# Optimization experiments

Measured on AMD Instinct MI355X. Metric: run time of the kernel, lower is better.

Reference implementation:

```python
import jax, jax.numpy as jnp
import numpy as np

USER_NUM = 100000
ITEM_NUM = 50000
E = 128   # embedding_size
A = 64    # attention_size
M = 8     # memory_size
B = 4096  # batch
NF = 50   # friends per user


def _l2norm(x, axis):
    # torch F.normalize(p=2): x / max(||x||, eps)
    n = jnp.sqrt(jnp.sum(x * x, axis=axis, keepdims=True))
    return x / jnp.maximum(n, 1e-12)


def setup_inputs() -> dict:
    key = jax.random.key(0)
    ks = jax.random.split(key, 9)
    u = lambda k, shape: jax.random.uniform(k, shape, jnp.float32, -0.1, 0.1)
    return {
        "input_u": jax.random.randint(ks[0], (B,), 0, USER_NUM),
        "input_i": jax.random.randint(ks[1], (B,), 0, ITEM_NUM),
        "input_uf": jax.random.randint(ks[2], (B, NF), 0, USER_NUM + 1),
        "uidW": u(ks[3], (USER_NUM + 1, E)),
        "iidW": u(ks[4], (ITEM_NUM, E)),
        "i_bias": jnp.zeros((ITEM_NUM,), jnp.float32),
        "Key": u(ks[5], (E, M)),
        "Mem": jnp.ones((M, E), jnp.float32),
        "WA": u(ks[6], (E, A)),
        "BA": jnp.zeros((A,), jnp.float32),
        "U_omega": u(ks[7], (A, 1)),
    }


def reference(input_u, input_i, input_uf, uidW, iidW, i_bias, Key, Mem, WA, BA, U_omega):
    user_num = uidW.shape[0] - 1  # padding id
    uid = uidW[input_u]                      # [B, E]
    iid = iidW[input_i]                      # [B, E]
    i_b = i_bias[input_i]                    # [B]
    fe = uidW[input_uf]                      # [B, F, E] friend embeddings
    fn = (input_uf != user_num).astype(uid.dtype)  # [B, F] valid-friend mask

    fe = fn[:, :, None] * fe
    uid_n = _l2norm(uid, axis=1)
    fe_n = _l2norm(fe, axis=2)
    cross = uid_n[:, None, :] * fe_n                     # [B, F, E]
    att_key = jnp.einsum('bfe,em->bfm', cross, Key)      # [B, F, M]
    att_mem = jax.nn.softmax(att_key, axis=0)            # softmax over batch (faithful to dim=0)
    att_mem = fn[:, :, None] * att_mem
    f1 = jnp.einsum('bfm,me->bfe', att_mem, Mem)         # [B, F, E]
    f2 = f1 * fe
    h = jax.nn.relu(jnp.einsum('bfe,ea->bfa', f2, WA) + BA)
    j = jnp.exp(jnp.einsum('bfa,ao->bfo', h, U_omega))   # [B, F, 1]
    j = fn[:, :, None] * j
    w = j / (jnp.sum(j, axis=1, keepdims=True) + 1e-8)
    friend = jnp.sum(w * f2, axis=1)                     # [B, E] (dropout p=0 -> identity)
    user = uid + friend
    score = jnp.sum(user * iid, axis=1) + i_b            # [B]
    return score
```

## Files before the change

kernel.cpp:

```cpp
#include <hip/hip_runtime.h>

#define EDIM 128
#define MDIM 8
#define ADIM 64
#define NFR  50
#define NCOL (NFR * MDIM)
#define NSLICE 64

typedef __attribute__((ext_vector_type(8))) short short8;
typedef __attribute__((ext_vector_type(4))) float f32x4;

__device__ __forceinline__ float waveReduceSum(float v) {
    #pragma unroll
    for (int s = 32; s >= 1; s >>= 1) v += __shfl_xor(v, s, 64);
    return v;
}
__device__ __forceinline__ short f2bf(float x) {
    unsigned u = __float_as_uint(x);
    u += 0x7FFFu + ((u >> 16) & 1u);
    return (short)(u >> 16);
}
__device__ __forceinline__ float bf2f(short s) {
    return __uint_as_float(((unsigned)(unsigned short)s) << 16);
}
__device__ __forceinline__ int fragOff(int r, int e) {
    int q = (e >> 3) & 3;
    int slot = (q * 16 + (r & 15)) ^ (q << 1);
    int block = ((r >> 4) << 2) | (e >> 5);
    return (block * 64 + slot) * 8;
}
__device__ __forceinline__ int slotR(int l) { return l ^ (((l >> 4) & 3) << 1); }

__global__ __launch_bounds__(256)
void k0_prep(const float* __restrict__ WA, const float* __restrict__ Key,
             short* __restrict__ WAfrag, short* __restrict__ Keyfrag,
             float* __restrict__ Ssum)
{
    int t = blockIdx.x * 256 + threadIdx.x;
    for (int i = t; i < NSLICE * NCOL; i += 5 * 256) Ssum[i] = 0.f;
    if (t < 1024) {
        int lane = t & 63;
        int Kt = (t >> 6) & 3;
        int Nt = t >> 8;
        int n  = Nt * 16 + (lane & 15);
        int k0 = Kt * 32 + (lane >> 4) * 8;
        short8 v;
        #pragma unroll
        for (int j = 0; j < 8; ++j) v[j] = f2bf(WA[(size_t)(k0 + j) * ADIM + n]);
        *(short8*)(WAfrag + (size_t)t * 8) = v;
    } else if (t < 1280) {
        int i = t - 1024;
        int lane = i & 63;
        int Kt = i >> 6;
        int n  = lane & 15;
        int k0 = Kt * 32 + (lane >> 4) * 8;
        short8 v;
        #pragma unroll
        for (int j = 0; j < 8; ++j)
            v[j] = (n < MDIM) ? f2bf(Key[(size_t)(k0 + j) * MDIM + n]) : (short)0;
        *(short8*)(Keyfrag + (size_t)i * 8) = v;
    }
}

__global__ __launch_bounds__(256, 2)
void k1_attkey(const int* __restrict__ input_u, const int* __restrict__ input_uf,
               const float* __restrict__ uidW, const short* __restrict__ Keyfrag,
               float* __restrict__ att_key, float* __restrict__ Ssum,
               int user_num, int B)
{
    __shared__ short crossF4[4][64 * EDIM];
    __shared__ float uidn4[4][EDIM];
    const int w = threadIdx.x >> 6, l = threadIdx.x & 63;
    const int b = blockIdx.x * 4 + w;
    if (b >= B) return;
    short* cF = crossF4[w];
    float* uidn = uidn4[w];

    const int u = input_u[b];
    int ufv = (l < NFR) ? input_uf[(size_t)b * NFR + l] : user_num;
    float x0 = uidW[(size_t)u * EDIM + l];
    float x1 = uidW[(size_t)u * EDIM + 64 + l];
    float s = waveReduceSum(x0 * x0 + x1 * x1);
    float uinv = 1.0f / fmaxf(sqrtf(s), 1e-12f);
    uidn[l] = x0 * uinv;
    uidn[64 + l] = x1 * uinv;
    __builtin_amdgcn_wave_barrier();

    const int kg = l & 15, fl = l >> 4;
    const int e0 = kg * 8;
    float4 un0 = *(const float4*)&uidn[e0];
    float4 un1 = *(const float4*)&uidn[e0 + 4];

    #pragma unroll 4
    for (int it = 0; it < 13; ++it) {
        int f = fl + 4 * it;
        short8 outv = {0, 0, 0, 0, 0, 0, 0, 0};
        if (f < NFR) {
            int fid = __shfl(ufv, f, 64);
            float fn = (fid != user_num) ? 1.f : 0.f;
            const float* fp = uidW + (size_t)fid * EDIM + e0;
            float4 g0 = *(const float4*)fp;
            float4 g1 = *(const float4*)(fp + 4);
            g0.x *= fn; g0.y *= fn; g0.z *= fn; g0.w *= fn;
            g1.x *= fn; g1.y *= fn; g1.z *= fn; g1.w *= fn;
            float fss = g0.x*g0.x + g0.y*g0.y + g0.z*g0.z + g0.w*g0.w
                      + g1.x*g1.x + g1.y*g1.y + g1.z*g1.z + g1.w*g1.w;
            fss += __shfl_xor(fss, 1, 64);
            fss += __shfl_xor(fss, 2, 64);
            fss += __shfl_xor(fss, 4, 64);
            fss += __shfl_xor(fss, 8, 64);
            float inv = 1.0f / fmaxf(sqrtf(fss), 1e-12f);
            outv[0] = f2bf(un0.x * g0.x * inv);
            outv[1] = f2bf(un0.y * g0.y * inv);
            outv[2] = f2bf(un0.z * g0.z * inv);
            outv[3] = f2bf(un0.w * g0.w * inv);
            outv[4] = f2bf(un1.x * g1.x * inv);
            outv[5] = f2bf(un1.y * g1.y * inv);
            outv[6] = f2bf(un1.z * g1.z * inv);
            outv[7] = f2bf(un1.w * g1.w * inv);
        }
        *(short8*)&cF[fragOff(f, e0)] = outv;
    }
    __builtin_amdgcn_wave_barrier();

    const int sl = slotR(l);
    f32x4 acc[4];
    #pragma unroll
    for (int Mt = 0; Mt < 4; ++Mt) acc[Mt] = (f32x4){0.f, 0.f, 0.f, 0.f};
    #pragma unroll
    for (int Kt = 0; Kt < 4; ++Kt) {
        short8 bf = *(const short8*)(Keyfrag + (size_t)(Kt * 64 + l) * 8);
        #pragma unroll
        for (int Mt = 0; Mt < 4; ++Mt) {
            short8 a = *(const short8*)&cF[(((Mt << 2) | Kt) * 64 + sl) * 8];
            acc[Mt] = __builtin_amdgcn_mfma_f32_16x16x32_bf16(a, bf, acc[Mt], 0, 0, 0);
        }
    }
    const int m = l & 15;
    if (m < MDIM) {
        float* Ss = Ssum + (size_t)(b & (NSLICE - 1)) * NCOL;
        #pragma unroll
        for (int Mt = 0; Mt < 4; ++Mt) {
            const int fbase = Mt * 16 + (l >> 4) * 4;
            #pragma unroll
            for (int r = 0; r < 4; ++r) {
                int f = fbase + r;
                if (f < NFR) {
                    att_key[((size_t)b * NFR + f) * MDIM + m] = acc[Mt][r];
                    atomicAdd(&Ss[f * MDIM + m], __expf(acc[Mt][r]));
                }
            }
        }
    }
}

__global__ __launch_bounds__(256)
void k2b_merge(const float* __restrict__ Ssum, float* __restrict__ ise)
{
    int col = blockIdx.x * 256 + threadIdx.x;
    if (col >= NCOL) return;
    float S = 0.f;
    #pragma unroll
    for (int s = 0; s < NSLICE; ++s) S += Ssum[s * NCOL + col];
    ise[col] = 1.0f / S;
}

__global__ __launch_bounds__(256, 2)
void k3_final(const int* __restrict__ input_u, const int* __restrict__ input_i,
              const int* __restrict__ input_uf, const float* __restrict__ uidW,
              const float* __restrict__ iidW, const float* __restrict__ i_bias,
              const float* __restrict__ Mem, const short* __restrict__ WAfrag,
              const float* __restrict__ BA, const float* __restrict__ U_omega,
              const float* __restrict__ att_key, const float* __restrict__ ise,
              float* __restrict__ out, int user_num, int B)
{
    __shared__ short f2F4[4][64 * EDIM];
    __shared__ float amL4[4][NCOL];
    __shared__ float jxL4[4][64];
    const int w = threadIdx.x >> 6, l = threadIdx.x & 63;
    const int b = blockIdx.x * 4 + w;
    if (b >= B) return;
    short* f2F = f2F4[w];
    float* amL = amL4[w];
    float* jxL = jxL4[w];

    const int u = input_u[b];
    const int ii = input_i[b];
    const float ib = i_bias[ii];
    int ufv = (l < NFR) ? input_uf[(size_t)b * NFR + l] : user_num;

    const int kg = l & 15, fl = l >> 4;
    const int e0 = kg * 8;

    #pragma unroll
    for (int c = 0; c < 7; ++c) {
        int i = l + 64 * c;
        if (i < NCOL) {
            float ak = att_key[(size_t)b * NCOL + i];
            int fid = __shfl(ufv, i >> 3, 64);
            amL[i] = (fid != user_num) ? __expf(ak) * ise[i] : 0.f;
        }
    }

    float4 mA[MDIM], mB[MDIM];
    #pragma unroll
    for (int m = 0; m < MDIM; ++m) {
        mA[m] = *(const float4*)&Mem[m * EDIM + e0];
        mB[m] = *(const float4*)&Mem[m * EDIM + e0 + 4];
    }
    __builtin_amdgcn_wave_barrier();

    #pragma unroll 4
    for (int it = 0; it < 16; ++it) {
        int f = fl + 4 * it;
        short8 outv = {0, 0, 0, 0, 0, 0, 0, 0};
        if (f < NFR) {
            int fid = __shfl(ufv, f, 64);
            const float* fp = uidW + (size_t)fid * EDIM + e0;
            float4 g0 = *(const float4*)fp;
            float4 g1 = *(const float4*)(fp + 4);
            float4 am0 = *(const float4*)&amL[f * 8];
            float4 am1 = *(const float4*)&amL[f * 8 + 4];
            float4 fa = {0.f, 0.f, 0.f, 0.f}, fb = {0.f, 0.f, 0.f, 0.f};
            #pragma unroll
            for (int m = 0; m < 4; ++m) {
                float c0 = (&am0.x)[m], c1 = (&am1.x)[m];
                fa.x += c0 * mA[m].x + c1 * mA[m + 4].x;
                fa.y += c0 * mA[m].y + c1 * mA[m + 4].y;
                fa.z += c0 * mA[m].z + c1 * mA[m + 4].z;
                fa.w += c0 * mA[m].w + c1 * mA[m + 4].w;
                fb.x += c0 * mB[m].x + c1 * mB[m + 4].x;
                fb.y += c0 * mB[m].y + c1 * mB[m + 4].y;
                fb.z += c0 * mB[m].z + c1 * mB[m + 4].z;
                fb.w += c0 * mB[m].w + c1 * mB[m + 4].w;
            }
            outv[0] = f2bf(fa.x * g0.x);
            outv[1] = f2bf(fa.y * g0.y);
            outv[2] = f2bf(fa.z * g0.z);
            outv[3] = f2bf(fa.w * g0.w);
            outv[4] = f2bf(fb.x * g1.x);
            outv[5] = f2bf(fb.y * g1.y);
            outv[6] = f2bf(fb.z * g1.z);
            outv[7] = f2bf(fb.w * g1.w);
        }
        *(short8*)&f2F[fragOff(f, e0)] = outv;
    }
    __builtin_amdgcn_wave_barrier();

    const int sl = slotR(l);
    f32x4 acc[4][4];
    #pragma unroll
    for (int Mt = 0; Mt < 4; ++Mt)
        #pragma unroll
        for (int Nt = 0; Nt < 4; ++Nt) acc[Mt][Nt] = (f32x4){0.f, 0.f, 0.f, 0.f};
    #pragma unroll
    for (int Kt = 0; Kt < 4; ++Kt) {
        short8 a[4];
        #pragma unroll
        for (int Mt = 0; Mt < 4; ++Mt)
            a[Mt] = *(const short8*)&f2F[(((Mt << 2) | Kt) * 64 + sl) * 8];
        #pragma unroll
        for (int Nt = 0; Nt < 4; ++Nt) {
            short8 bf = *(const short8*)(WAfrag + (size_t)(((Nt << 2) | Kt) * 64 + l) * 8);
            #pragma unroll
            for (int Mt = 0; Mt < 4; ++Mt)
                acc[Mt][Nt] = __builtin_amdgcn_mfma_f32_16x16x32_bf16(a[Mt], bf, acc[Mt][Nt], 0, 0, 0);
        }
    }

    float ba4[4], uo4[4];
    #pragma unroll
    for (int Nt = 0; Nt < 4; ++Nt) {
        ba4[Nt] = BA[Nt * 16 + kg];
        uo4[Nt] = U_omega[Nt * 16 + kg];
    }
    float v[16];
    #pragma unroll
    for (int Mt = 0; Mt < 4; ++Mt)
        #pragma unroll
        for (int r = 0; r < 4; ++r) {
            float sv = 0.f;
            #pragma unroll
            for (int Nt = 0; Nt < 4; ++Nt)
                sv += fmaxf(acc[Mt][Nt][r] + ba4[Nt], 0.f) * uo4[Nt];
            v[Mt * 4 + r] = sv;
        }

    const bool c0 = l & 1, c1 = l & 2, c2 = l & 4, c3 = l & 8;
    #pragma unroll
    for (int k = 0; k < 8; ++k) {
        float lo = v[k], hi = v[k + 8];
        float send = c0 ? lo : hi;
        float recv = __shfl_xor(send, 1, 64);
        v[k] = c0 ? (hi + recv) : (lo + recv);
    }
    #pragma unroll
    for (int k = 0; k < 4; ++k) {
        float lo = v[k], hi = v[k + 4];
        float send = c1 ? lo : hi;
        float recv = __shfl_xor(send, 2, 64);
        v[k] = c1 ? (hi + recv) : (lo + recv);
    }
    #pragma unroll
    for (int k = 0; k < 2; ++k) {
        float lo = v[k], hi = v[k + 2];
        float send = c2 ? lo : hi;
        float recv = __shfl_xor(send, 4, 64);
        v[k] = c2 ? (hi + recv) : (lo + recv);
    }
    {
        float lo = v[0], hi = v[1];
        float send = c3 ? lo : hi;
        float recv = __shfl_xor(send, 8, 64);
        v[0] = c3 ? (hi + recv) : (lo + recv);
    }
    const int vIdx = ((l & 1) << 3) | ((l & 2) << 1) | ((l & 4) >> 1) | ((l & 8) >> 3);
    const int fLane = (vIdx >> 2) * 16 + (l >> 4) * 4 + (vIdx & 3);

    int ufF = __shfl(ufv, fLane, 64);
    float jv = 0.f;
    if (fLane < NFR && ufF != user_num) jv = __expf(v[0]);
    jxL[fLane] = jv;
    float winv = 1.0f / (waveReduceSum(jv) + 1e-8f);
    __builtin_amdgcn_wave_barrier();

    float pa[8] = {0.f, 0.f, 0.f, 0.f, 0.f, 0.f, 0.f, 0.f};
    #pragma unroll 4
    for (int it = 0; it < 16; ++it) {
        int f = fl + 4 * it;
        float jf = jxL[f];
        short8 vv = *(const short8*)&f2F[fragOff(f, e0)];
        #pragma unroll
        for (int j = 0; j < 8; ++j) pa[j] += jf * bf2f(vv[j]);
    }
    #pragma unroll
    for (int j = 0; j < 8; ++j) {
        pa[j] += __shfl_xor(pa[j], 16, 64);
        pa[j] += __shfl_xor(pa[j], 32, 64);
    }

    const float* up = uidW + (size_t)u * EDIM + e0;
    const float* ip = iidW + (size_t)ii * EDIM + e0;
    float4 u0 = *(const float4*)up;
    float4 u1 = *(const float4*)(up + 4);
    float4 i0 = *(const float4*)ip;
    float4 i1 = *(const float4*)(ip + 4);
    float sc = 0.f;
    #pragma unroll
    for (int j = 0; j < 4; ++j) {
        sc += ((&u0.x)[j] + pa[j] * winv) * (&i0.x)[j];
        sc += ((&u1.x)[j] + pa[j + 4] * winv) * (&i1.x)[j];
    }
    float red = waveReduceSum(sc);
    if (l == 0) out[b] = red * 0.25f + ib;
}

extern "C" void kernel_launch(void* const* d_in, const int* in_sizes, int n_in,
                              void* d_out, int out_size, void* d_ws, size_t ws_size,
                              hipStream_t stream)
{
    const int*   input_u  = (const int*)d_in[0];
    const int*   input_i  = (const int*)d_in[1];
    const int*   input_uf = (const int*)d_in[2];
    const float* uidW     = (const float*)d_in[3];
    const float* iidW     = (const float*)d_in[4];
    const float* i_bias   = (const float*)d_in[5];
    const float* Key      = (const float*)d_in[6];
    const float* Mem      = (const float*)d_in[7];
    const float* WA       = (const float*)d_in[8];
    const float* BA       = (const float*)d_in[9];
    const float* U_om     = (const float*)d_in[10];

    const int B = in_sizes[0];
    const int user_num = in_sizes[3] / EDIM - 1;

    float* att  = (float*)d_ws;
    float* Ssum = att + (size_t)B * NCOL;
    float* ise  = Ssum + NSLICE * NCOL;
    short* WAfrag  = (short*)(ise + NCOL);
    short* Keyfrag = WAfrag + 4 * 4 * 64 * 8;

    const int nb = (B + 3) / 4;
    k0_prep<<<5, 256, 0, stream>>>(WA, Key, WAfrag, Keyfrag, Ssum);
    k1_attkey<<<nb, 256, 0, stream>>>(input_u, input_uf, uidW, Keyfrag, att,
                                      Ssum, user_num, B);
    k2b_merge<<<2, 256, 0, stream>>>(Ssum, ise);
    k3_final<<<nb, 256, 0, stream>>>(input_u, input_i, input_uf, uidW, iidW, i_bias,
                                     Mem, WAfrag, BA, U_om, att, ise,
                                     (float*)d_out, user_num, B);
}
```

Baseline: 173.0 us.

## Stage friend embeddings into LDS asynchronously and pipeline compute per tile

Both k1 and k3 now issue global_load_lds async copies of all 50 friend embedding rows into a swizzled LDS buffer up front. Compute then proceeds in four stages, each gated by a partial vmcnt wait, so normalisation, bf16 packing and MFMA overlap with the remaining loads. Blocks shrink to one wave per batch row, and k3 stages Mem through LDS while k1 hoists the Key fragments into registers. This increases LDS per wave (about 25 KB in k1 and more in k3), which may limit occupancy, and it relies on hand-counted vmcnt values being correct.

Result: slower. 203.3 us (+17.5%).

```diff
diff --git a/kernel.cpp b/kernel.cpp
--- a/kernel.cpp
+++ b/kernel.cpp
@@ -10,6 +10,15 @@
 typedef __attribute__((ext_vector_type(8))) short short8;
 typedef __attribute__((ext_vector_type(4))) float f32x4;
 
+#define WAITVM(N) do { asm volatile("s_waitcnt vmcnt(" #N ")" ::: "memory"); \
+                       __builtin_amdgcn_sched_barrier(0); } while (0)
+
+__device__ __forceinline__ void asyncStage16(const void* g, void* l) {
+    __builtin_amdgcn_global_load_lds(
+        (const __attribute__((address_space(1))) void*)g,
+        (__attribute__((address_space(3))) void*)l, 16, 0, 0);
+}
+
 __device__ __forceinline__ float waveReduceSum(float v) {
     #pragma unroll
     for (int s = 32; s >= 1; s >>= 1) v += __shfl_xor(v, s, 64);
@@ -30,6 +39,7 @@
     return (block * 64 + slot) * 8;
 }
 __device__ __forceinline__ int slotR(int l) { return l ^ (((l >> 4) & 3) << 1); }
+
 
 __global__ __launch_bounds__(256)
 void k0_prep(const float* __restrict__ WA, const float* __restrict__ Key,
@@ -62,82 +72,105 @@
     }
 }
 
-__global__ __launch_bounds__(256, 2)
+__global__ __launch_bounds__(64)
 void k1_attkey(const int* __restrict__ input_u, const int* __restrict__ input_uf,
                const float* __restrict__ uidW, const short* __restrict__ Keyfrag,
                float* __restrict__ att_key, float* __restrict__ Ssum,
-               int user_num, int B)
+               int user_num)
 {
-    __shared__ short crossF4[4][64 * EDIM];
-    __shared__ float uidn4[4][EDIM];
-    const int w = threadIdx.x >> 6, l = threadIdx.x & 63;
-    const int b = blockIdx.x * 4 + w;
-    if (b >= B) return;
-    short* cF = crossF4[w];
-    float* uidn = uidn4[w];
+    __shared__ float rawFe[NFR * EDIM];
+    __shared__ float uidn[EDIM];
+    const int l = threadIdx.x;
+    const int b = blockIdx.x;
 
     const int u = input_u[b];
     int ufv = (l < NFR) ? input_uf[(size_t)b * NFR + l] : user_num;
     float x0 = uidW[(size_t)u * EDIM + l];
     float x1 = uidW[(size_t)u * EDIM + 64 + l];
+    short8 kb[4];
+    #pragma unroll
+    for (int Kt = 0; Kt < 4; ++Kt)
+        kb[Kt] = *(const short8*)(Keyfrag + (size_t)(Kt * 64 + l) * 8);
+
     float s = waveReduceSum(x0 * x0 + x1 * x1);
     float uinv = 1.0f / fmaxf(sqrtf(s), 1e-12f);
     uidn[l] = x0 * uinv;
     uidn[64 + l] = x1 * uinv;
     __builtin_amdgcn_wave_barrier();
 
-    const int kg = l & 15, fl = l >> 4;
-    const int e0 = kg * 8;
-    float4 un0 = *(const float4*)&uidn[e0];
-    float4 un1 = *(const float4*)&uidn[e0 + 4];
-
-    #pragma unroll 4
-    for (int it = 0; it < 13; ++it) {
-        int f = fl + 4 * it;
-        short8 outv = {0, 0, 0, 0, 0, 0, 0, 0};
-        if (f < NFR) {
+    asm volatile("s_waitcnt vmcnt(0)" ::: "memory");
+    __builtin_amdgcn_sched_barrier(0);
+
+    {
+        const int half = l >> 5, i = l & 31;
+        #pragma unroll
+        for (int c = 0; c < 25; ++c) {
+            int f = 2 * c + half;
             int fid = __shfl(ufv, f, 64);
-            float fn = (fid != user_num) ? 1.f : 0.f;
-            const float* fp = uidW + (size_t)fid * EDIM + e0;
-            float4 g0 = *(const float4*)fp;
-            float4 g1 = *(const float4*)(fp + 4);
-            g0.x *= fn; g0.y *= fn; g0.z *= fn; g0.w *= fn;
-            g1.x *= fn; g1.y *= fn; g1.z *= fn; g1.w *= fn;
-            float fss = g0.x*g0.x + g0.y*g0.y + g0.z*g0.z + g0.w*g0.w
-                      + g1.x*g1.x + g1.y*g1.y + g1.z*g1.z + g1.w*g1.w;
-            fss += __shfl_xor(fss, 1, 64);
-            fss += __shfl_xor(fss, 2, 64);
-            fss += __shfl_xor(fss, 4, 64);
-            fss += __shfl_xor(fss, 8, 64);
-            float inv = 1.0f / fmaxf(sqrtf(fss), 1e-12f);
-            outv[0] = f2bf(un0.x * g0.x * inv);
-            outv[1] = f2bf(un0.y * g0.y * inv);
-            outv[2] = f2bf(un0.z * g0.z * inv);
-            outv[3] = f2bf(un0.w * g0.w * inv);
-            outv[4] = f2bf(un1.x * g1.x * inv);
-            outv[5] = f2bf(un1.y * g1.y * inv);
-            outv[6] = f2bf(un1.z * g1.z * inv);
-            outv[7] = f2bf(un1.w * g1.w * inv);
-        }
-        *(short8*)&cF[fragOff(f, e0)] = outv;
-    }
-    __builtin_amdgcn_wave_barrier();
-
-    const int sl = slotR(l);
-    f32x4 acc[4];
-    #pragma unroll
-    for (int Mt = 0; Mt < 4; ++Mt) acc[Mt] = (f32x4){0.f, 0.f, 0.f, 0.f};
+            const char* g = (const char*)(uidW + (size_t)fid * EDIM)
+                          + ((i * 16) ^ ((f & 7) << 4));
+            asyncStage16(g, (char*)rawFe + c * 1024);
+        }
+    }
+    __builtin_amdgcn_sched_barrier(0);
+
+    const int ko = (l >> 4) * 8;
+    float4 unA[4], unB[4];
     #pragma unroll
     for (int Kt = 0; Kt < 4; ++Kt) {
-        short8 bf = *(const short8*)(Keyfrag + (size_t)(Kt * 64 + l) * 8);
-        #pragma unroll
-        for (int Mt = 0; Mt < 4; ++Mt) {
-            short8 a = *(const short8*)&cF[(((Mt << 2) | Kt) * 64 + sl) * 8];
-            acc[Mt] = __builtin_amdgcn_mfma_f32_16x16x32_bf16(a, bf, acc[Mt], 0, 0, 0);
-        }
-    }
-    const int m = l & 15;
-    if (m < MDIM) {
+        unA[Kt] = *(const float4*)&uidn[Kt * 32 + ko];
+        unB[Kt] = *(const float4*)&uidn[Kt * 32 + ko + 4];
+    }
+
+    const int fr = l & 15;
+    f32x4 accM[4];
+
+    auto doMt = [&](int Mt) {
+        int f = Mt * 16 + fr;
+        int fc = (f < NFR) ? f : 0;
+        int sw = (fc & 7) << 4;
+        const char* rp = (const char*)rawFe + fc * 512;
+        float4 fea[4], feb[4];
+        #pragma unroll
+        for (int Kt = 0; Kt < 4; ++Kt) {
+            int base = Kt * 128 + (l >> 4) * 32;
+            fea[Kt] = *(const float4*)(rp + (base ^ sw));
+            feb[Kt] = *(const float4*)(rp + ((base + 16) ^ sw));
+        }
+        float fss = 0.f;
+        #pragma unroll
+        for (int Kt = 0; Kt < 4; ++Kt)
+            fss += fea[Kt].x*fea[Kt].x + fea[Kt].y*fea[Kt].y
+                 + fea[Kt].z*fea[Kt].z + fea[Kt].w*fea[Kt].w
+                 + feb[Kt].x*feb[Kt].x + feb[Kt].y*feb[Kt].y
+                 + feb[Kt].z*feb[Kt].z + feb[Kt].w*feb[Kt].w;
+        fss += __shfl_xor(fss, 16, 64);
+        fss += __shfl_xor(fss, 32, 64);
+        int fid = __shfl(ufv, fc, 64);
+        float fn = (f < NFR && fid != user_num) ? 1.f : 0.f;
+        float inv = fn / fmaxf(sqrtf(fss), 1e-12f);
+        f32x4 acc = {0.f, 0.f, 0.f, 0.f};
+        #pragma unroll
+        for (int Kt = 0; Kt < 4; ++Kt) {
+            short8 a;
+            a[0] = f2bf(unA[Kt].x * fea[Kt].x * inv);
+            a[1] = f2bf(unA[Kt].y * fea[Kt].y * inv);
+            a[2] = f2bf(unA[Kt].z * fea[Kt].z * inv);
+            a[3] = f2bf(unA[Kt].w * fea[Kt].w * inv);
+            a[4] = f2bf(unB[Kt].x * feb[Kt].x * inv);
+            a[5] = f2bf(unB[Kt].y * feb[Kt].y * inv);
+            a[6] = f2bf(unB[Kt].z * feb[Kt].z * inv);
+            a[7] = f2bf(unB[Kt].w * feb[Kt].w * inv);
+            acc = __builtin_amdgcn_mfma_f32_16x16x32_bf16(a, kb[Kt], acc, 0, 0, 0);
+        }
+        accM[Mt] = acc;
+    };
+    WAITVM(17); doMt(0);
+    WAITVM(9);  doMt(1);
+    WAITVM(1);  doMt(2);
+    WAITVM(0);  doMt(3);
+
+    if (fr < MDIM) {
         float* Ss = Ssum + (size_t)(b & (NSLICE - 1)) * NCOL;
         #pragma unroll
         for (int Mt = 0; Mt < 4; ++Mt) {
@@ -146,8 +179,8 @@
             for (int r = 0; r < 4; ++r) {
                 int f = fbase + r;
                 if (f < NFR) {
-                    att_key[((size_t)b * NFR + f) * MDIM + m] = acc[Mt][r];
-                    atomicAdd(&Ss[f * MDIM + m], __expf(acc[Mt][r]));
+                    att_key[((size_t)b * NFR + f) * MDIM + fr] = accM[Mt][r];
+                    atomicAdd(&Ss[f * MDIM + fr], __expf(accM[Mt][r]));
                 }
             }
         }
@@ -165,74 +198,97 @@
     ise[col] = 1.0f / S;
 }
 
-__global__ __launch_bounds__(256, 2)
+__global__ __launch_bounds__(64)
 void k3_final(const int* __restrict__ input_u, const int* __restrict__ input_i,
               const int* __restrict__ input_uf, const float* __restrict__ uidW,
               const float* __restrict__ iidW, const float* __restrict__ i_bias,
               const float* __restrict__ Mem, const short* __restrict__ WAfrag,
               const float* __restrict__ BA, const float* __restrict__ U_omega,
               const float* __restrict__ att_key, const float* __restrict__ ise,
-              float* __restrict__ out, int user_num, int B)
+              float* __restrict__ out, int user_num)
 {
-    __shared__ short f2F4[4][64 * EDIM];
-    __shared__ float amL4[4][NCOL];
-    __shared__ float jxL4[4][64];
-    const int w = threadIdx.x >> 6, l = threadIdx.x & 63;
-    const int b = blockIdx.x * 4 + w;
-    if (b >= B) return;
-    short* f2F = f2F4[w];
-    float* amL = amL4[w];
-    float* jxL = jxL4[w];
+    __shared__ float rawFe[NFR * EDIM];
+    __shared__ short f2F[64 * EDIM];
+    __shared__ float amL[NCOL];
+    __shared__ float MemL[MDIM * EDIM];
+    __shared__ float jxL[64];
+    const int l = threadIdx.x;
+    const int b = blockIdx.x;
 
     const int u = input_u[b];
     const int ii = input_i[b];
     const float ib = i_bias[ii];
     int ufv = (l < NFR) ? input_uf[(size_t)b * NFR + l] : user_num;
 
-    const int kg = l & 15, fl = l >> 4;
-    const int e0 = kg * 8;
-
+    float akv[7], isv[7];
+    #pragma unroll
+    for (int c = 0; c < 7; ++c) {
+        int i = l + 64 * c;
+        if (i < NCOL) { akv[c] = att_key[(size_t)b * NCOL + i]; isv[c] = ise[i]; }
+    }
+    #pragma unroll
+    for (int c = 0; c < 2; ++c) {
+        int i = l + 64 * c;
+        float4 v = *(const float4*)&Mem[i * 4];
+        *(float4*)&MemL[i * 4] = v;
+    }
     #pragma unroll
     for (int c = 0; c < 7; ++c) {
         int i = l + 64 * c;
         if (i < NCOL) {
-            float ak = att_key[(size_t)b * NCOL + i];
             int fid = __shfl(ufv, i >> 3, 64);
-            amL[i] = (fid != user_num) ? __expf(ak) * ise[i] : 0.f;
-        }
-    }
-
-    float4 mA[MDIM], mB[MDIM];
+            amL[i] = (fid != user_num) ? __expf(akv[c]) * isv[c] : 0.f;
+        }
+    }
+    __builtin_amdgcn_wave_barrier();
+
+    asm volatile("s_waitcnt vmcnt(0)" ::: "memory");
+    __builtin_amdgcn_sched_barrier(0);
+
+    {
+        const int half = l >> 5, i = l & 31;
+        #pragma unroll
+        for (int c = 0; c < 25; ++c) {
+            int f = 2 * c + half;
+            int fid = __shfl(ufv, f, 64);
+            const char* g = (const char*)(uidW + (size_t)fid * EDIM)
+                          + ((i * 16) ^ ((f & 7) << 4));
+            asyncStage16(g, (char*)rawFe + c * 1024);
+        }
+    }
+    __builtin_amdgcn_sched_barrier(0);
+
+    const int kg = l & 15, fl = l >> 4;
+    const int e0 = kg * 8;
+    float4 mAv[MDIM], mBv[MDIM];
     #pragma unroll
     for (int m = 0; m < MDIM; ++m) {
-        mA[m] = *(const float4*)&Mem[m * EDIM + e0];
-        mB[m] = *(const float4*)&Mem[m * EDIM + e0 + 4];
-    }
-    __builtin_amdgcn_wave_barrier();
-
-    #pragma unroll 4
-    for (int it = 0; it < 16; ++it) {
+        mAv[m] = *(const float4*)&MemL[m * EDIM + e0];
+        mBv[m] = *(const float4*)&MemL[m * EDIM + e0 + 4];
+    }
+
+    auto doIt = [&](int it) {
         int f = fl + 4 * it;
         short8 outv = {0, 0, 0, 0, 0, 0, 0, 0};
         if (f < NFR) {
-            int fid = __shfl(ufv, f, 64);
-            const float* fp = uidW + (size_t)fid * EDIM + e0;
-            float4 g0 = *(const float4*)fp;
-            float4 g1 = *(const float4*)(fp + 4);
+            int sw = (f & 7) << 4;
+            const char* rp = (const char*)rawFe + f * 512;
+            float4 g0 = *(const float4*)(rp + ((e0 * 4) ^ sw));
+            float4 g1 = *(const float4*)(rp + ((e0 * 4 + 16) ^ sw));
             float4 am0 = *(const float4*)&amL[f * 8];
             float4 am1 = *(const float4*)&amL[f * 8 + 4];
             float4 fa = {0.f, 0.f, 0.f, 0.f}, fb = {0.f, 0.f, 0.f, 0.f};
             #pragma unroll
             for (int m = 0; m < 4; ++m) {
                 float c0 = (&am0.x)[m], c1 = (&am1.x)[m];
-                fa.x += c0 * mA[m].x + c1 * mA[m + 4].x;
-                fa.y += c0 * mA[m].y + c1 * mA[m + 4].y;
-                fa.z += c0 * mA[m].z + c1 * mA[m + 4].z;
-                fa.w += c0 * mA[m].w + c1 * mA[m + 4].w;
-                fb.x += c0 * mB[m].x + c1 * mB[m + 4].x;
-                fb.y += c0 * mB[m].y + c1 * mB[m + 4].y;
-                fb.z += c0 * mB[m].z + c1 * mB[m + 4].z;
-                fb.w += c0 * mB[m].w + c1 * mB[m + 4].w;
+                fa.x += c0 * mAv[m].x + c1 * mAv[m + 4].x;
+                fa.y += c0 * mAv[m].y + c1 * mAv[m + 4].y;
+                fa.z += c0 * mAv[m].z + c1 * mAv[m + 4].z;
+                fa.w += c0 * mAv[m].w + c1 * mAv[m + 4].w;
+                fb.x += c0 * mBv[m].x + c1 * mBv[m + 4].x;
+                fb.y += c0 * mBv[m].y + c1 * mBv[m + 4].y;
+                fb.z += c0 * mBv[m].z + c1 * mBv[m + 4].z;
+                fb.w += c0 * mBv[m].w + c1 * mBv[m + 4].w;
             }
             outv[0] = f2bf(fa.x * g0.x);
             outv[1] = f2bf(fa.y * g0.y);
@@ -244,7 +300,11 @@
             outv[7] = f2bf(fb.w * g1.w);
         }
         *(short8*)&f2F[fragOff(f, e0)] = outv;
-    }
+    };
+    WAITVM(17); doIt(0);  doIt(1);  doIt(2);  doIt(3);
+    WAITVM(9);  doIt(4);  doIt(5);  doIt(6);  doIt(7);
+    WAITVM(1);  doIt(8);  doIt(9);  doIt(10); doIt(11);
+    WAITVM(0);  doIt(12); doIt(13); doIt(14); doIt(15);
     __builtin_amdgcn_wave_barrier();
 
     const int sl = slotR(l);
@@ -380,12 +440,11 @@
     short* WAfrag  = (short*)(ise + NCOL);
     short* Keyfrag = WAfrag + 4 * 4 * 64 * 8;
 
-    const int nb = (B + 3) / 4;
     k0_prep<<<5, 256, 0, stream>>>(WA, Key, WAfrag, Keyfrag, Ssum);
-    k1_attkey<<<nb, 256, 0, stream>>>(input_u, input_uf, uidW, Keyfrag, att,
-                                      Ssum, user_num, B);
+    k1_attkey<<<B, 64, 0, stream>>>(input_u, input_uf, uidW, Keyfrag, att,
+                                    Ssum, user_num);
     k2b_merge<<<2, 256, 0, stream>>>(Ssum, ise);
-    k3_final<<<nb, 256, 0, stream>>>(input_u, input_i, input_uf, uidW, iidW, i_bias,
-                                     Mem, WAfrag, BA, U_om, att, ise,
-                                     (float*)d_out, user_num, B);
-}
+    k3_final<<<B, 64, 0, stream>>>(input_u, input_i, input_uf, uidW, iidW, i_bias,
+                                   Mem, WAfrag, BA, U_om, att, ise,
+                                   (float*)d_out, user_num);
+}
```

## Fold user norm into Key and apply friend norm after MFMA in attkey

Applied to the files above, without the earlier changes.

The attention-key kernel no longer builds the normalized cross product in shared memory. It scales the Key fragment by the normalized user embedding and feeds raw friend embeddings straight from global memory into the MFMA as the A operand. The friend L2 norm and the validity mask are applied afterwards as a per-row scale on the accumulator. Blocks shrink to one wavefront per batch row, which removes the large LDS tile and allows more resident waves, at the cost of extra bf16 rounding of the scaled Key and of the unnormalized friend values.

Result: no change. 173.0 us (+0.0%).

```diff
diff --git a/kernel.cpp b/kernel.cpp
--- a/kernel.cpp
+++ b/kernel.cpp
@@ -62,80 +62,86 @@
     }
 }
 
-__global__ __launch_bounds__(256, 2)
+__global__ __launch_bounds__(64)
 void k1_attkey(const int* __restrict__ input_u, const int* __restrict__ input_uf,
                const float* __restrict__ uidW, const short* __restrict__ Keyfrag,
                float* __restrict__ att_key, float* __restrict__ Ssum,
-               int user_num, int B)
-{
-    __shared__ short crossF4[4][64 * EDIM];
-    __shared__ float uidn4[4][EDIM];
-    const int w = threadIdx.x >> 6, l = threadIdx.x & 63;
-    const int b = blockIdx.x * 4 + w;
-    if (b >= B) return;
-    short* cF = crossF4[w];
-    float* uidn = uidn4[w];
+               int user_num)
+{
+    __shared__ float uidn[EDIM];
+    __shared__ float invL[64];
+    const int l = threadIdx.x;
+    const int b = blockIdx.x;
 
     const int u = input_u[b];
     int ufv = (l < NFR) ? input_uf[(size_t)b * NFR + l] : user_num;
     float x0 = uidW[(size_t)u * EDIM + l];
     float x1 = uidW[(size_t)u * EDIM + 64 + l];
+
+    int fid[4];
+    #pragma unroll
+    for (int Mt = 0; Mt < 4; ++Mt)
+        fid[Mt] = __shfl(ufv, Mt * 16 + (l & 15), 64);
+    const int eo = (l >> 4) * 8;
+
     float s = waveReduceSum(x0 * x0 + x1 * x1);
     float uinv = 1.0f / fmaxf(sqrtf(s), 1e-12f);
     uidn[l] = x0 * uinv;
     uidn[64 + l] = x1 * uinv;
     __builtin_amdgcn_wave_barrier();
 
-    const int kg = l & 15, fl = l >> 4;
-    const int e0 = kg * 8;
-    float4 un0 = *(const float4*)&uidn[e0];
-    float4 un1 = *(const float4*)&uidn[e0 + 4];
-
-    #pragma unroll 4
-    for (int it = 0; it < 13; ++it) {
-        int f = fl + 4 * it;
-        short8 outv = {0, 0, 0, 0, 0, 0, 0, 0};
-        if (f < NFR) {
-            int fid = __shfl(ufv, f, 64);
-            float fn = (fid != user_num) ? 1.f : 0.f;
-            const float* fp = uidW + (size_t)fid * EDIM + e0;
-            float4 g0 = *(const float4*)fp;
-            float4 g1 = *(const float4*)(fp + 4);
-            g0.x *= fn; g0.y *= fn; g0.z *= fn; g0.w *= fn;
-            g1.x *= fn; g1.y *= fn; g1.z *= fn; g1.w *= fn;
-            float fss = g0.x*g0.x + g0.y*g0.y + g0.z*g0.z + g0.w*g0.w
-                      + g1.x*g1.x + g1.y*g1.y + g1.z*g1.z + g1.w*g1.w;
-            fss += __shfl_xor(fss, 1, 64);
-            fss += __shfl_xor(fss, 2, 64);
-            fss += __shfl_xor(fss, 4, 64);
-            fss += __shfl_xor(fss, 8, 64);
-            float inv = 1.0f / fmaxf(sqrtf(fss), 1e-12f);
-            outv[0] = f2bf(un0.x * g0.x * inv);
-            outv[1] = f2bf(un0.y * g0.y * inv);
-            outv[2] = f2bf(un0.z * g0.z * inv);
-            outv[3] = f2bf(un0.w * g0.w * inv);
-            outv[4] = f2bf(un1.x * g1.x * inv);
-            outv[5] = f2bf(un1.y * g1.y * inv);
-            outv[6] = f2bf(un1.z * g1.z * inv);
-            outv[7] = f2bf(un1.w * g1.w * inv);
-        }
-        *(short8*)&cF[fragOff(f, e0)] = outv;
-    }
-    __builtin_amdgcn_wave_barrier();
-
-    const int sl = slotR(l);
     f32x4 acc[4];
     #pragma unroll
     for (int Mt = 0; Mt < 4; ++Mt) acc[Mt] = (f32x4){0.f, 0.f, 0.f, 0.f};
+    float fss[4] = {0.f, 0.f, 0.f, 0.f};
+
     #pragma unroll
     for (int Kt = 0; Kt < 4; ++Kt) {
-        short8 bf = *(const short8*)(Keyfrag + (size_t)(Kt * 64 + l) * 8);
+        float4 ga[4], gb[4];
         #pragma unroll
         for (int Mt = 0; Mt < 4; ++Mt) {
-            short8 a = *(const short8*)&cF[(((Mt << 2) | Kt) * 64 + sl) * 8];
-            acc[Mt] = __builtin_amdgcn_mfma_f32_16x16x32_bf16(a, bf, acc[Mt], 0, 0, 0);
-        }
-    }
+            const float* fp = uidW + (size_t)fid[Mt] * EDIM + Kt * 32 + eo;
+            ga[Mt] = *(const float4*)fp;
+            gb[Mt] = *(const float4*)(fp + 4);
+        }
+        short8 kb = *(const short8*)(Keyfrag + (size_t)(Kt * 64 + l) * 8);
+        float4 un0 = *(const float4*)&uidn[Kt * 32 + eo];
+        float4 un1 = *(const float4*)&uidn[Kt * 32 + eo + 4];
+        short8 kbp;
+        kbp[0] = f2bf(un0.x * bf2f(kb[0]));
+        kbp[1] = f2bf(un0.y * bf2f(kb[1]));
+        kbp[2] = f2bf(un0.z * bf2f(kb[2]));
+        kbp[3] = f2bf(un0.w * bf2f(kb[3]));
+        kbp[4] = f2bf(un1.x * bf2f(kb[4]));
+        kbp[5] = f2bf(un1.y * bf2f(kb[5]));
+        kbp[6] = f2bf(un1.z * bf2f(kb[6]));
+        kbp[7] = f2bf(un1.w * bf2f(kb[7]));
+        #pragma unroll
+        for (int Mt = 0; Mt < 4; ++Mt) {
+            fss[Mt] += ga[Mt].x*ga[Mt].x + ga[Mt].y*ga[Mt].y
+                     + ga[Mt].z*ga[Mt].z + ga[Mt].w*ga[Mt].w
+                     + gb[Mt].x*gb[Mt].x + gb[Mt].y*gb[Mt].y
+                     + gb[Mt].z*gb[Mt].z + gb[Mt].w*gb[Mt].w;
+            short8 a;
+            a[0] = f2bf(ga[Mt].x); a[1] = f2bf(ga[Mt].y);
+            a[2] = f2bf(ga[Mt].z); a[3] = f2bf(ga[Mt].w);
+            a[4] = f2bf(gb[Mt].x); a[5] = f2bf(gb[Mt].y);
+            a[6] = f2bf(gb[Mt].z); a[7] = f2bf(gb[Mt].w);
+            acc[Mt] = __builtin_amdgcn_mfma_f32_16x16x32_bf16(a, kbp, acc[Mt], 0, 0, 0);
+        }
+    }
+
+    #pragma unroll
+    for (int Mt = 0; Mt < 4; ++Mt) {
+        float t = fss[Mt];
+        t += __shfl_xor(t, 16, 64);
+        t += __shfl_xor(t, 32, 64);
+        int f = Mt * 16 + (l & 15);
+        float fn = (f < NFR && fid[Mt] != user_num) ? 1.f : 0.f;
+        invL[f] = fn / fmaxf(sqrtf(t), 1e-12f);
+    }
+    __builtin_amdgcn_wave_barrier();
+
     const int m = l & 15;
     if (m < MDIM) {
         float* Ss = Ssum + (size_t)(b & (NSLICE - 1)) * NCOL;
@@ -146,8 +152,9 @@
             for (int r = 0; r < 4; ++r) {
                 int f = fbase + r;
                 if (f < NFR) {
-                    att_key[((size_t)b * NFR + f) * MDIM + m] = acc[Mt][r];
-                    atomicAdd(&Ss[f * MDIM + m], __expf(acc[Mt][r]));
+                    float val = acc[Mt][r] * invL[f];
+                    att_key[((size_t)b * NFR + f) * MDIM + m] = val;
+                    atomicAdd(&Ss[f * MDIM + m], __expf(val));
                 }
             }
         }
@@ -382,8 +389,8 @@
 
     const int nb = (B + 3) / 4;
     k0_prep<<<5, 256, 0, stream>>>(WA, Key, WAfrag, Keyfrag, Ssum);
-    k1_attkey<<<nb, 256, 0, stream>>>(input_u, input_uf, uidW, Keyfrag, att,
-                                      Ssum, user_num, B);
+    k1_attkey<<<B, 64, 0, stream>>>(input_u, input_uf, uidW, Keyfrag, att,
+                                    Ssum, user_num);
     k2b_merge<<<2, 256, 0, stream>>>(Ssum, ise);
     k3_final<<<nb, 256, 0, stream>>>(input_u, input_i, input_uf, uidW, iidW, i_bias,
                                      Mem, WAfrag, BA, U_om, att, ise,
```
